# Optimization experiments

Measured on AMD Instinct MI355X. Metric: run time of the kernel, lower is better.

The kernel has to match this reference:

```python
import jax, jax.numpy as jnp
import numpy as np

B, N, GN, GS = 16, 100000, 4096, 64  # batch, points, num_groups, group_size


def setup_inputs() -> dict:
    key = jax.random.key(0)
    k1, k2, k3 = jax.random.split(key, 3)
    x_proto = jax.random.normal(k1, (B, N, 3), dtype=jnp.float32)
    template = jax.random.normal(k2, (N, 3), dtype=jnp.float32)
    groups = jax.random.randint(k3, (GN, GS), 0, N, dtype=jnp.int32)
    return {"x_proto": x_proto, "template": template, "groups": groups}


def reference(x_proto, template, groups):
    # x_proto: [B, N, 3], template: [N, 3], groups: [GN, GS] int indices
    b, n, _ = x_proto.shape
    Yg = template[groups]                      # [GN, GS, 3] gathered template
    Xg = x_proto[:, groups]                    # [B, GN, GS, 3] gathered current points

    # Kabsch: align template group Y to current X (R @ Y + t ~ X)
    muY = Yg.mean(axis=1)                      # [GN, 3]
    muX = Xg.mean(axis=2)                      # [B, GN, 3]
    Yc = Yg - muY[:, None, :]
    Xc = Xg - muX[:, :, None, :]
    H = jnp.einsum('gni,bgnj->bgij', Yc, Xc)   # [B, GN, 3, 3] covariance
    U, S, Vh = jnp.linalg.svd(H)
    V = jnp.swapaxes(Vh, -2, -1)
    R0 = V @ jnp.swapaxes(U, -2, -1)
    det = jnp.linalg.det(R0)                   # [B, GN]
    # flip last column of V where det < 0 to get a proper rotation
    s = jnp.where(det < 0, -1.0, 1.0).astype(x_proto.dtype)
    col_scale = jnp.stack([jnp.ones_like(s), jnp.ones_like(s), s], axis=-1)  # [B, GN, 3]
    R = (V * col_scale[..., None, :]) @ jnp.swapaxes(U, -2, -1)              # [B, GN, 3, 3]
    t = muX - jnp.einsum('bgij,gj->bgi', R, muY)                             # [B, GN, 3]

    # project template group through (R, t)
    Xg_proj = jnp.einsum('bgij,gnj->bgni', R, Yg) + t[:, :, None, :]         # [B, GN, GS, 3]

    # scatter-add with overlap counting, then average
    flat_idx = groups.reshape(-1)              # [GN*GS]
    out = jnp.zeros_like(x_proto).at[:, flat_idx].add(Xg_proj.reshape(b, -1, 3))
    counts = jnp.zeros((n,), dtype=x_proto.dtype).at[flat_idx].add(1.0)
    counts = jnp.maximum(counts, 1.0)
    return out / counts[None, :, None]
```

## Files before the change

### kernel.cpp

```cpp
#include <hip/hip_runtime.h>
#include <math.h>

static constexpr int BB = 16;
static constexpr int NN = 100000;
static constexpr int GN = 4096;
static constexpr int GS = 64;
static constexpr int NP = BB * GN;
static constexpr int NE = GN * GS;
static constexpr int NBLK = (NN + 255) / 256;

__device__ __forceinline__ float wsum64(float v) {
#pragma unroll
  for (int off = 32; off > 0; off >>= 1) v += __shfl_xor(v, off, 64);
  return v;
}

__global__ __launch_bounds__(256) void k_zero(
    int4* __restrict__ cnt4, int* __restrict__ gtotal) {
  int t = blockIdx.x * 256 + threadIdx.x;
  if (t == 0) *gtotal = 0;
  if (t < NN / 4) cnt4[t] = make_int4(0, 0, 0, 0);
}

__global__ __launch_bounds__(256) void k_tpl(
    const float* __restrict__ tpl, const int* __restrict__ groups,
    float* __restrict__ Yg, float* __restrict__ GmY,
    int* __restrict__ cnt, int* __restrict__ epos) {
  int g    = blockIdx.x * 4 + (threadIdx.x >> 6);
  int lane = threadIdx.x & 63;
  int e    = g * GS + lane;
  int idx = groups[e];
  int pos = atomicAdd(&cnt[idx], 1);
  epos[e] = pos;
  float3 y = *(const float3*)(tpl + (size_t)idx * 3);
  float* o = Yg + ((size_t)g * GS + lane) * 3;
  o[0] = y.x; o[1] = y.y; o[2] = y.z;
  float sy0 = wsum64(y.x), sy1 = wsum64(y.y), sy2 = wsum64(y.z);
  if (lane == 0) {
    const float inv = 1.0f / 64.0f;
    *(float4*)(GmY + (size_t)g * 4) =
        make_float4(sy0 * inv, sy1 * inv, sy2 * inv, 0.0f);
  }
}

__global__ __launch_bounds__(256) void k_stats(
    const float* __restrict__ x, const float* __restrict__ Yg,
    const float* __restrict__ GmY, const int* __restrict__ groups,
    float* __restrict__ Ht) {
  int bid  = (blockIdx.x & 7) * 512 + (blockIdx.x >> 3);
  int wid4 = bid * 4 + (threadIdx.x >> 6);
  int lane = threadIdx.x & 63;
  int s    = lane >> 4;
  int l4   = lane & 15;
  int p = wid4 * 4 + s;
  int b = p >> 12;
  int g = p & (GN - 1);

  int4 iv = *(const int4*)(groups + (size_t)g * GS + l4 * 4);
  const float4* yv = (const float4*)(Yg + ((size_t)g * GS + l4 * 4) * 3);
  float4 ya = yv[0], yb = yv[1], yc = yv[2];

  const float* xb = x + (size_t)b * NN * 3;
  float sx0 = 0.f, sx1 = 0.f, sx2 = 0.f;
  float h00 = 0.f, h01 = 0.f, h02 = 0.f;
  float h10 = 0.f, h11 = 0.f, h12 = 0.f;
  float h20 = 0.f, h21 = 0.f, h22 = 0.f;

#define ACC(Y0, Y1, Y2, IDX)                                   \
  {                                                            \
    float3 xv = *(const float3*)(xb + (size_t)(IDX) * 3);      \
    sx0 += xv.x; sx1 += xv.y; sx2 += xv.z;                     \
    h00 += (Y0) * xv.x; h01 += (Y0) * xv.y; h02 += (Y0) * xv.z;\
    h10 += (Y1) * xv.x; h11 += (Y1) * xv.y; h12 += (Y1) * xv.z;\
    h20 += (Y2) * xv.x; h21 += (Y2) * xv.y; h22 += (Y2) * xv.z;\
  }
  ACC(ya.x, ya.y, ya.z, iv.x);
  ACC(ya.w, yb.x, yb.y, iv.y);
  ACC(yb.z, yb.w, yc.x, iv.z);
  ACC(yc.y, yc.z, yc.w, iv.w);
#undef ACC

#define RED(V)                                                 \
  V += __shfl_xor(V, 8, 64); V += __shfl_xor(V, 4, 64);        \
  V += __shfl_xor(V, 2, 64); V += __shfl_xor(V, 1, 64);
  RED(sx0) RED(sx1) RED(sx2)
  RED(h00) RED(h01) RED(h02)
  RED(h10) RED(h11) RED(h12)
  RED(h20) RED(h21) RED(h22)
#undef RED

  if (l4 == 0) {
    const float inv = 1.0f / 64.0f;
    float4 m = *(const float4*)(GmY + (size_t)g * 4);
    float mx0 = sx0 * inv, mx1 = sx1 * inv, mx2 = sx2 * inv;
    float4 o0 = make_float4(mx0, mx1, mx2, h00 - m.x * sx0);
    float4 o1 = make_float4(h01 - m.x * sx1, h02 - m.x * sx2,
                            h10 - m.y * sx0, h11 - m.y * sx1);
    float4 o2 = make_float4(h12 - m.y * sx2, h20 - m.z * sx0,
                            h21 - m.z * sx1, h22 - m.z * sx2);
    float* o = Ht + (size_t)p * 12;
    *(float4*)(o + 0) = o0;
    *(float4*)(o + 4) = o1;
    *(float4*)(o + 8) = o2;
  }
}

#define JROT(P, Q, RR)                                                        \
  {                                                                           \
    float apq = K[P][Q];                                                      \
    if (fabsf(apq) > 1e-30f) {                                                \
      float app = K[P][P], aqq = K[Q][Q];                                     \
      float tau = (aqq - app) / (2.0f * apq);                                 \
      float tt = copysignf(1.0f, tau) / (fabsf(tau) + sqrtf(1.0f + tau*tau)); \
      float cc = 1.0f / sqrtf(1.0f + tt * tt);                                \
      float ss = tt * cc;                                                     \
      K[P][P] = app - tt * apq;                                               \
      K[Q][Q] = aqq + tt * apq;                                               \
      K[P][Q] = 0.0f; K[Q][P] = 0.0f;                                         \
      float krp = K[RR][P], krq = K[RR][Q];                                   \
      K[RR][P] = cc * krp - ss * krq; K[P][RR] = K[RR][P];                    \
      K[RR][Q] = ss * krp + cc * krq; K[Q][RR] = K[RR][Q];                    \
      float v0p = V[0][P], v0q = V[0][Q];                                     \
      float v1p = V[1][P], v1q = V[1][Q];                                     \
      float v2p = V[2][P], v2q = V[2][Q];                                     \
      V[0][P] = cc * v0p - ss * v0q; V[0][Q] = ss * v0p + cc * v0q;           \
      V[1][P] = cc * v1p - ss * v1q; V[1][Q] = ss * v1p + cc * v1q;           \
      V[2][P] = cc * v2p - ss * v2q; V[2][Q] = ss * v2p + cc * v2q;           \
    }                                                                         \
  }

#define FIN(AA, BBi, CC)                                                      \
  {                                                                           \
    float va0 = V[0][AA], va1 = V[1][AA], va2 = V[2][AA];                     \
    float vb0 = V[0][BBi], vb1 = V[1][BBi], vb2 = V[2][BBi];                  \
    float vc0 = V[0][CC], vc1 = V[1][CC], vc2 = V[2][CC];                     \
    float ua0 = A[0][0]*va0 + A[0][1]*va1 + A[0][2]*va2;                      \
    float ua1 = A[1][0]*va0 + A[1][1]*va1 + A[1][2]*va2;                      \
    float ua2 = A[2][0]*va0 + A[2][1]*va1 + A[2][2]*va2;                      \
    float il = 1.0f / sqrtf(ua0*ua0 + ua1*ua1 + ua2*ua2 + 1e-30f);            \
    ua0 *= il; ua1 *= il; ua2 *= il;                                          \
    float ub0 = A[0][0]*vb0 + A[0][1]*vb1 + A[0][2]*vb2;                      \
    float ub1 = A[1][0]*vb0 + A[1][1]*vb1 + A[1][2]*vb2;                      \
    float ub2 = A[2][0]*vb0 + A[2][1]*vb1 + A[2][2]*vb2;                      \
    il = 1.0f / sqrtf(ub0*ub0 + ub1*ub1 + ub2*ub2 + 1e-30f);                  \
    ub0 *= il; ub1 *= il; ub2 *= il;                                          \
    float dd = ua0*ub0 + ua1*ub1 + ua2*ub2;                                   \
    ub0 -= dd * ua0; ub1 -= dd * ua1; ub2 -= dd * ua2;                        \
    il = 1.0f / sqrtf(ub0*ub0 + ub1*ub1 + ub2*ub2 + 1e-30f);                  \
    ub0 *= il; ub1 *= il; ub2 *= il;                                          \
    float uc0 = ua1*ub2 - ua2*ub1;                                            \
    float uc1 = ua2*ub0 - ua0*ub2;                                            \
    float uc2 = ua0*ub1 - ua1*ub0;                                            \
    R[0][0] = va0*ua0 + vb0*ub0 + dsg*vc0*uc0;                                \
    R[0][1] = va0*ua1 + vb0*ub1 + dsg*vc0*uc1;                                \
    R[0][2] = va0*ua2 + vb0*ub2 + dsg*vc0*uc2;                                \
    R[1][0] = va1*ua0 + vb1*ub0 + dsg*vc1*uc0;                                \
    R[1][1] = va1*ua1 + vb1*ub1 + dsg*vc1*uc1;                                \
    R[1][2] = va1*ua2 + vb1*ub2 + dsg*vc1*uc2;                                \
    R[2][0] = va2*ua0 + vb2*ub0 + dsg*vc2*uc0;                                \
    R[2][1] = va2*ua1 + vb2*ub1 + dsg*vc2*uc1;                                \
    R[2][2] = va2*ua2 + vb2*ub2 + dsg*vc2*uc2;                                \
  }

__global__ __launch_bounds__(256) void k_svd(
    const float* __restrict__ Ht, const float* __restrict__ GmY,
    float* __restrict__ Qt) {
  int p = blockIdx.x * 256 + threadIdx.x;
  if (p >= NP) return;
  int g = p & (GN - 1);
  const float* h = Ht + (size_t)p * 12;
  float4 f0 = *(const float4*)(h + 0);
  float4 f1 = *(const float4*)(h + 4);
  float4 f2 = *(const float4*)(h + 8);
  float4 m  = *(const float4*)(GmY + (size_t)g * 4);
  float mx0 = f0.x, mx1 = f0.y, mx2 = f0.z;
  float my0 = m.x, my1 = m.y, my2 = m.z;
  float A[3][3];
  A[0][0] = f0.w; A[0][1] = f1.x; A[0][2] = f1.y;
  A[1][0] = f1.z; A[1][1] = f1.w; A[1][2] = f2.x;
  A[2][0] = f2.y; A[2][1] = f2.z; A[2][2] = f2.w;

  float K[3][3];
#pragma unroll
  for (int i = 0; i < 3; ++i)
#pragma unroll
    for (int j = 0; j < 3; ++j)
      K[i][j] = A[0][i]*A[0][j] + A[1][i]*A[1][j] + A[2][i]*A[2][j];

  float V[3][3] = {{1.f,0.f,0.f},{0.f,1.f,0.f},{0.f,0.f,1.f}};
#pragma unroll
  for (int sweep = 0; sweep < 5; ++sweep) {
    JROT(0, 1, 2);
    JROT(0, 2, 1);
    JROT(1, 2, 0);
  }

  float d0 = K[0][0], d1 = K[1][1], d2 = K[2][2];
  float detV = V[0][0]*(V[1][1]*V[2][2] - V[1][2]*V[2][1])
             - V[0][1]*(V[1][0]*V[2][2] - V[1][2]*V[2][0])
             + V[0][2]*(V[1][0]*V[2][1] - V[1][1]*V[2][0]);
  float dsg = (detV < 0.0f) ? -1.0f : 1.0f;

  float R[3][3];
  if (d0 <= d1 && d0 <= d2) {
    FIN(1, 2, 0);
  } else if (d1 <= d0 && d1 <= d2) {
    FIN(2, 0, 1);
  } else {
    FIN(0, 1, 2);
  }

  float t0 = mx0 - (R[0][0]*my0 + R[0][1]*my1 + R[0][2]*my2);
  float t1 = mx1 - (R[1][0]*my0 + R[1][1]*my1 + R[1][2]*my2);
  float t2 = mx2 - (R[2][0]*my0 + R[2][1]*my1 + R[2][2]*my2);

  float qw, qx, qy, qz;
  float tr = R[0][0] + R[1][1] + R[2][2];
  if (tr > 0.f) {
    float S = sqrtf(tr + 1.0f) * 2.0f;
    qw = 0.25f * S;
    qx = (R[2][1] - R[1][2]) / S;
    qy = (R[0][2] - R[2][0]) / S;
    qz = (R[1][0] - R[0][1]) / S;
  } else if (R[0][0] > R[1][1] && R[0][0] > R[2][2]) {
    float S = sqrtf(1.0f + R[0][0] - R[1][1] - R[2][2]) * 2.0f;
    qw = (R[2][1] - R[1][2]) / S;
    qx = 0.25f * S;
    qy = (R[0][1] + R[1][0]) / S;
    qz = (R[0][2] + R[2][0]) / S;
  } else if (R[1][1] > R[2][2]) {
    float S = sqrtf(1.0f + R[1][1] - R[0][0] - R[2][2]) * 2.0f;
    qw = (R[0][2] - R[2][0]) / S;
    qx = (R[0][1] + R[1][0]) / S;
    qy = 0.25f * S;
    qz = (R[1][2] + R[2][1]) / S;
  } else {
    float S = sqrtf(1.0f + R[2][2] - R[0][0] - R[1][1]) * 2.0f;
    qw = (R[1][0] - R[0][1]) / S;
    qx = (R[0][2] + R[2][0]) / S;
    qy = (R[1][2] + R[2][1]) / S;
    qz = 0.25f * S;
  }
  float il2 = 1.0f / sqrtf(qw*qw + qx*qx + qy*qy + qz*qz);
  qw *= il2; qx *= il2; qy *= il2; qz *= il2;

  float* o = Qt + (size_t)p * 8;
  *(float4*)(o + 0) = make_float4(qx, qy, qz, qw);
  *(float4*)(o + 4) = make_float4(t0, t1, t2, 0.f);
}

__global__ __launch_bounds__(256) void k_alloc(
    const int* __restrict__ cnt, int* __restrict__ gtotal,
    int2* __restrict__ rs_cnt, int* __restrict__ entries) {
  int t = blockIdx.x * 256 + threadIdx.x;
  int lane = threadIdx.x & 63;
  int v  = (t < NN) ? cnt[t] : 0;
  int vp = (v + 3) & ~3;
  int sc = vp;
#pragma unroll
  for (int off = 1; off < 64; off <<= 1) {
    int u = __shfl_up(sc, off, 64);
    if (lane >= off) sc += u;
  }
  int wtotal = __shfl(sc, 63, 64);
  int base = 0;
  if (lane == 63) base = atomicAdd(gtotal, wtotal);
  base = __shfl(base, 63, 64);
  if (t < NN) {
    int s = base + sc - vp;
    rs_cnt[t] = make_int2(s, v);
    for (int k = v; k < vp; ++k) entries[s + k] = 0;
  }
}

__global__ __launch_bounds__(256) void k_fill(
    const int* __restrict__ groups, const int2* __restrict__ rs_cnt,
    const int* __restrict__ epos, int* __restrict__ entries) {
  int e = blockIdx.x * 256 + threadIdx.x;
  if (e >= NE) return;
  int n = groups[e];
  entries[rs_cnt[n].x + epos[e]] = e >> 6;
}

__global__ __launch_bounds__(256) void k_gather(
    const float* __restrict__ tpl, const int2* __restrict__ rs_cnt,
    const int* __restrict__ entries, const float* __restrict__ Qt,
    float* __restrict__ out) {
  int bid = blockIdx.x;
  int xcd = bid & 7;
  int i   = bid >> 3;
  int b   = xcd * 2 + (i / NBLK);
  int nb  = i % NBLK;
  int n   = nb * 256 + threadIdx.x;
  if (n >= NN) return;
  int2 rc = rs_cnt[n];
  int s = rc.x, c = rc.y;
  float3 y = *(const float3*)(tpl + (size_t)n * 3);
  float p0 = 0.f, p1 = 0.f, p2 = 0.f;
  const float* Qb = Qt + (size_t)b * GN * 8;

  for (int j = 0; j < c; j += 4) {
    int4 ev = *(const int4*)(entries + s + j);
    const float* qp0 = Qb + (size_t)ev.x * 8;
    const float* qp1 = Qb + (size_t)ev.y * 8;
    const float* qp2 = Qb + (size_t)ev.z * 8;
    const float* qp3 = Qb + (size_t)ev.w * 8;
    float4 qa = *(const float4*)(qp0);
    float4 ta = *(const float4*)(qp0 + 4);
    float4 qb = *(const float4*)(qp1);
    float4 tb = *(const float4*)(qp1 + 4);
    float4 qc = *(const float4*)(qp2);
    float4 tc = *(const float4*)(qp2 + 4);
    float4 qd = *(const float4*)(qp3);
    float4 td = *(const float4*)(qp3 + 4);
#define QACC(Q, T, K)                                                   \
    {                                                                   \
      float w = (j + (K) < c) ? 1.f : 0.f;                              \
      float tx = 2.f * ((Q).y * y.z - (Q).z * y.y);                     \
      float ty = 2.f * ((Q).z * y.x - (Q).x * y.z);                     \
      float tz = 2.f * ((Q).x * y.y - (Q).y * y.x);                     \
      p0 += w * (y.x + (Q).w * tx + ((Q).y * tz - (Q).z * ty) + (T).x); \
      p1 += w * (y.y + (Q).w * ty + ((Q).z * tx - (Q).x * tz) + (T).y); \
      p2 += w * (y.z + (Q).w * tz + ((Q).x * ty - (Q).y * tx) + (T).z); \
    }
    QACC(qa, ta, 0)
    QACC(qb, tb, 1)
    QACC(qc, tc, 2)
    QACC(qd, td, 3)
#undef QACC
  }
  float inv = 1.0f / fmaxf((float)c, 1.0f);
  float* o = out + ((size_t)b * NN + (size_t)n) * 3;
  *(float3*)o = make_float3(p0 * inv, p1 * inv, p2 * inv);
}

extern "C" void kernel_launch(void* const* d_in, const int* in_sizes, int n_in,
                              void* d_out, int out_size, void* d_ws, size_t ws_size,
                              hipStream_t stream) {
  const float* x      = (const float*)d_in[0];
  const float* tpl    = (const float*)d_in[1];
  const int*   groups = (const int*)d_in[2];
  float* out = (float*)d_out;

  char* ws = (char*)d_ws;
  size_t o_yg   = 0;
  size_t o_ht   = o_yg + 3145728;
  size_t o_qt   = o_ht + 3145728;
  size_t o_gmy  = o_qt + 2097152;
  size_t o_cnt  = o_gmy + 65536;
  size_t o_rsc  = o_cnt + 400000;
  size_t o_gt   = o_rsc + 800000;
  size_t o_epos = o_gt + 64;
  size_t o_ent  = o_epos + 1048576;
  float* Yg     = (float*)(ws + o_yg);
  float* Ht     = (float*)(ws + o_ht);
  float* Qt     = (float*)(ws + o_qt);
  float* GmY    = (float*)(ws + o_gmy);
  int*   cnt    = (int*)(ws + o_cnt);
  int2*  rs_cnt = (int2*)(ws + o_rsc);
  int*   gtotal = (int*)(ws + o_gt);
  int*   epos   = (int*)(ws + o_epos);
  int*   entries= (int*)(ws + o_ent);

  k_zero<<<(NN / 4 + 255) / 256, 256, 0, stream>>>((int4*)cnt, gtotal);
  k_tpl<<<GN / 4, 256, 0, stream>>>(tpl, groups, Yg, GmY, cnt, epos);
  k_stats<<<NP / 16, 256, 0, stream>>>(x, Yg, GmY, groups, Ht);
  k_svd<<<NP / 256, 256, 0, stream>>>(Ht, GmY, Qt);
  k_alloc<<<NBLK, 256, 0, stream>>>(cnt, gtotal, rs_cnt, entries);
  k_fill<<<NE / 256, 256, 0, stream>>>(groups, rs_cnt, epos, entries);
  k_gather<<<8 * 2 * NBLK, 256, 0, stream>>>(tpl, rs_cnt, entries, Qt, out);
}
```

Baseline: 122.5 us.

## Stage per-batch quaternion table in LDS for gather, drop entry padding

```diff
diff --git a/kernel.cpp b/kernel.cpp
--- a/kernel.cpp
+++ b/kernel.cpp
@@ -8,6 +8,7 @@
 static constexpr int NP = BB * GN;
 static constexpr int NE = GN * GS;
 static constexpr int NBLK = (NN + 255) / 256;
+static constexpr int GNB = (NN + 1023) / 1024;
 
 __device__ __forceinline__ float wsum64(float v) {
 #pragma unroll
@@ -251,12 +252,11 @@
 
 __global__ __launch_bounds__(256) void k_alloc(
     const int* __restrict__ cnt, int* __restrict__ gtotal,
-    int2* __restrict__ rs_cnt, int* __restrict__ entries) {
+    int2* __restrict__ rs_cnt) {
   int t = blockIdx.x * 256 + threadIdx.x;
   int lane = threadIdx.x & 63;
   int v  = (t < NN) ? cnt[t] : 0;
-  int vp = (v + 3) & ~3;
-  int sc = vp;
+  int sc = v;
 #pragma unroll
   for (int off = 1; off < 64; off <<= 1) {
     int u = __shfl_up(sc, off, 64);
@@ -266,11 +266,7 @@
   int base = 0;
   if (lane == 63) base = atomicAdd(gtotal, wtotal);
   base = __shfl(base, 63, 64);
-  if (t < NN) {
-    int s = base + sc - vp;
-    rs_cnt[t] = make_int2(s, v);
-    for (int k = v; k < vp; ++k) entries[s + k] = 0;
-  }
+  if (t < NN) rs_cnt[t] = make_int2(base + sc - v, v);
 }
 
 __global__ __launch_bounds__(256) void k_fill(
@@ -282,52 +278,37 @@
   entries[rs_cnt[n].x + epos[e]] = e >> 6;
 }
 
-__global__ __launch_bounds__(256) void k_gather(
+__global__ __launch_bounds__(1024, 1) void k_gather(
     const float* __restrict__ tpl, const int2* __restrict__ rs_cnt,
-    const int* __restrict__ entries, const float* __restrict__ Qt,
+    const int* __restrict__ entries, const float4* __restrict__ Qt4,
     float* __restrict__ out) {
-  int bid = blockIdx.x;
-  int xcd = bid & 7;
-  int i   = bid >> 3;
-  int b   = xcd * 2 + (i / NBLK);
-  int nb  = i % NBLK;
-  int n   = nb * 256 + threadIdx.x;
+  __shared__ float4 sq[GN];
+  __shared__ float4 st[GN];
+  int b = blockIdx.y;
+  const float4* Qb = Qt4 + (size_t)b * GN * 2;
+  for (int j = threadIdx.x; j < GN * 2; j += 1024) {
+    float4 v = Qb[j];
+    if (j & 1) st[j >> 1] = v;
+    else       sq[j >> 1] = v;
+  }
+  __syncthreads();
+
+  int n = blockIdx.x * 1024 + threadIdx.x;
   if (n >= NN) return;
   int2 rc = rs_cnt[n];
   int s = rc.x, c = rc.y;
   float3 y = *(const float3*)(tpl + (size_t)n * 3);
   float p0 = 0.f, p1 = 0.f, p2 = 0.f;
-  const float* Qb = Qt + (size_t)b * GN * 8;
-
-  for (int j = 0; j < c; j += 4) {
-    int4 ev = *(const int4*)(entries + s + j);
-    const float* qp0 = Qb + (size_t)ev.x * 8;
-    const float* qp1 = Qb + (size_t)ev.y * 8;
-    const float* qp2 = Qb + (size_t)ev.z * 8;
-    const float* qp3 = Qb + (size_t)ev.w * 8;
-    float4 qa = *(const float4*)(qp0);
-    float4 ta = *(const float4*)(qp0 + 4);
-    float4 qb = *(const float4*)(qp1);
-    float4 tb = *(const float4*)(qp1 + 4);
-    float4 qc = *(const float4*)(qp2);
-    float4 tc = *(const float4*)(qp2 + 4);
-    float4 qd = *(const float4*)(qp3);
-    float4 td = *(const float4*)(qp3 + 4);
-#define QACC(Q, T, K)                                                   \
-    {                                                                   \
-      float w = (j + (K) < c) ? 1.f : 0.f;                              \
-      float tx = 2.f * ((Q).y * y.z - (Q).z * y.y);                     \
-      float ty = 2.f * ((Q).z * y.x - (Q).x * y.z);                     \
-      float tz = 2.f * ((Q).x * y.y - (Q).y * y.x);                     \
-      p0 += w * (y.x + (Q).w * tx + ((Q).y * tz - (Q).z * ty) + (T).x); \
-      p1 += w * (y.y + (Q).w * ty + ((Q).z * tx - (Q).x * tz) + (T).y); \
-      p2 += w * (y.z + (Q).w * tz + ((Q).x * ty - (Q).y * tx) + (T).z); \
-    }
-    QACC(qa, ta, 0)
-    QACC(qb, tb, 1)
-    QACC(qc, tc, 2)
-    QACC(qd, td, 3)
-#undef QACC
+  for (int j = 0; j < c; ++j) {
+    int g = entries[s + j];
+    float4 q  = sq[g];
+    float4 tv = st[g];
+    float tx = 2.f * (q.y * y.z - q.z * y.y);
+    float ty = 2.f * (q.z * y.x - q.x * y.z);
+    float tz = 2.f * (q.x * y.y - q.y * y.x);
+    p0 += y.x + q.w * tx + (q.y * tz - q.z * ty) + tv.x;
+    p1 += y.y + q.w * ty + (q.z * tx - q.x * tz) + tv.y;
+    p2 += y.z + q.w * tz + (q.x * ty - q.y * tx) + tv.z;
   }
   float inv = 1.0f / fmaxf((float)c, 1.0f);
   float* o = out + ((size_t)b * NN + (size_t)n) * 3;
@@ -366,7 +347,8 @@
   k_tpl<<<GN / 4, 256, 0, stream>>>(tpl, groups, Yg, GmY, cnt, epos);
   k_stats<<<NP / 16, 256, 0, stream>>>(x, Yg, GmY, groups, Ht);
   k_svd<<<NP / 256, 256, 0, stream>>>(Ht, GmY, Qt);
-  k_alloc<<<NBLK, 256, 0, stream>>>(cnt, gtotal, rs_cnt, entries);
+  k_alloc<<<NBLK, 256, 0, stream>>>(cnt, gtotal, rs_cnt);
   k_fill<<<NE / 256, 256, 0, stream>>>(groups, rs_cnt, epos, entries);
-  k_gather<<<8 * 2 * NBLK, 256, 0, stream>>>(tpl, rs_cnt, entries, Qt, out);
-}
+  k_gather<<<dim3(GNB, BB), 1024, 0, stream>>>(
+      tpl, rs_cnt, entries, (const float4*)Qt, out);
+}
```

New measurement: 122.7 us. About the same (+0.2%).
